# Performance work log

Hardware: AMD Instinct MI355X
Metric: run time of the kernel (lower is better)

The kernel has to match this reference:

```python
import jax, jax.numpy as jnp
import numpy as np

H = 512

def setup_inputs() -> dict:
    key = jax.random.key(0)
    ks = jax.random.split(key, 8)
    b, s, m, n, h = 8, 128, 32, 64, H
    sc = 1.0 / np.sqrt(h)
    return {
        "x": jax.random.normal(ks[0], (b, s, m, h), dtype=jnp.float32),
        "y": jax.random.normal(ks[1], (b, s, n, h), dtype=jnp.float32),
        # MultiHeadSelfAtt (additive self-attentive pooling: b*m*h -> b*h)
        "Wa1": jax.random.normal(ks[2], (h, h), dtype=jnp.float32) * sc,
        "ba1": jnp.zeros((h,), dtype=jnp.float32),
        "wa2": jax.random.normal(ks[3], (h,), dtype=jnp.float32) * sc,
        # gate Linear(2h -> h), torch layout weight: (h, 2h)
        "Wl": jax.random.normal(ks[4], (h, 2 * h), dtype=jnp.float32) * (1.0 / np.sqrt(2 * h)),
        "bl": jnp.zeros((h,), dtype=jnp.float32),
    }

def reference(x, y, Wa1, ba1, wa2, Wl, bl):
    h = x.shape[-1]
    # attentive pooling over m for every (b, s) slice: b s m h -> b s h
    scores = jnp.tanh(x @ Wa1 + ba1) @ wa2          # b s m
    attn = jax.nn.softmax(scores, axis=-1)
    pooled = jnp.einsum('bsm,bsmh->bsh', attn, x)   # b s h
    # step i (i>=1) uses pooled x at step i-1
    i_x = pooled[:, :-1]                            # b (s-1) h
    Wy, Wi = Wl[:, :h], Wl[:, h:]                   # split concat-linear
    pre = jnp.einsum('bsnh,gh->bsng', y[:, 1:], Wy) \
        + (i_x @ Wi.T + bl)[:, :, None, :]          # b (s-1) n h
    gate = jax.nn.sigmoid(pre)
    out_rest = y[:, 1:] + i_x[:, :, None, :] * gate
    return jnp.concatenate([y[:, :1], out_rest], axis=1)  # b s n h
```

## Files before the change

### kernel.cpp

```cpp
#include <hip/hip_runtime.h>
#include <cstdint>
#include <cstddef>

#define H 512
#define SEQ 128

typedef __bf16 v8bf __attribute__((ext_vector_type(8)));
typedef float v4f __attribute__((ext_vector_type(4)));
typedef unsigned short v8us __attribute__((ext_vector_type(8)));

__device__ __forceinline__ unsigned short f2bf(float f) {
    unsigned int u = __float_as_uint(f);
    u = (u + 0x7FFFu + ((u >> 16) & 1u)) >> 16;
    return (unsigned short)u;
}
__device__ __forceinline__ float bf2f(unsigned short h) {
    return __uint_as_float(((unsigned int)h) << 16);
}
__device__ __forceinline__ v8bf load_bf8(const unsigned short* p) {
    return *reinterpret_cast<const v8bf*>(p);
}
__device__ __forceinline__ float fast_tanh(float v) {
    float e = __expf(2.f * v);
    return 1.f - 2.f * __builtin_amdgcn_rcpf(e + 1.f);
}
__device__ __forceinline__ float fast_sigmoid(float v) {
    return __builtin_amdgcn_rcpf(1.f + __expf(-v));
}
__device__ __forceinline__ v8us cvt8u(float4 lo, float4 hi) {
    v8us r;
    r[0] = f2bf(lo.x); r[1] = f2bf(lo.y); r[2] = f2bf(lo.z); r[3] = f2bf(lo.w);
    r[4] = f2bf(hi.x); r[5] = f2bf(hi.y); r[6] = f2bf(hi.z); r[7] = f2bf(hi.w);
    return r;
}
__device__ __forceinline__ void gll16(const unsigned short* g, unsigned short* l) {
    __builtin_amdgcn_global_load_lds(
        (const __attribute__((address_space(1))) unsigned int*)g,
        (__attribute__((address_space(3))) unsigned int*)l, 16, 0, 0);
}


__global__ __launch_bounds__(256) void prep_kernel(
        const float* __restrict__ Wa1, const float* __restrict__ Wl,
        unsigned short* __restrict__ WyS, unsigned short* __restrict__ WiS,
        unsigned short* __restrict__ WaS) {
    int tg = blockIdx.x * 256 + threadIdx.x;
    int mat = tg >> 15;
    int idx = tg & 32767;
    int lane = idx & 63;
    int ks = (idx >> 6) & 15;
    int c = idx >> 10;
    int g = c * 16 + (lane & 15);
    int hb = ks * 32 + ((lane >> 4) << 3);
    unsigned short o[8];
    unsigned short* dst;
    if (mat == 0) {
        const float* s = Wl + (size_t)g * 1024 + hb;
#pragma unroll
        for (int j = 0; j < 8; ++j) o[j] = f2bf(s[j]);
        dst = WyS + (size_t)idx * 8;
    } else if (mat == 1) {
        const float* s = Wl + (size_t)g * 1024 + 512 + hb;
#pragma unroll
        for (int j = 0; j < 8; ++j) o[j] = f2bf(s[j]);
        dst = WiS + (size_t)idx * 8;
    } else {
#pragma unroll
        for (int j = 0; j < 8; ++j) o[j] = f2bf(Wa1[(size_t)(hb + j) * H + g]);
        dst = WaS + (size_t)idx * 8;
    }
    *reinterpret_cast<ushort4*>(dst)     = *reinterpret_cast<ushort4*>(&o[0]);
    *reinterpret_cast<ushort4*>(dst + 4) = *reinterpret_cast<ushort4*>(&o[4]);
}

__global__ __launch_bounds__(256, 4) void attn_pool_kernel(
        const float* __restrict__ x, const unsigned short* __restrict__ WaS,
        const float* __restrict__ ba1, const float* __restrict__ wa2,
        float* __restrict__ ixf, unsigned short* __restrict__ ixb) {
    __shared__ __align__(16) unsigned short Xb[32][520];
    __shared__ float attn[32];
    __shared__ float scpart[4][32];

    int bid = blockIdx.x;
    int b = bid / 127, s = bid % 127;
    int t = threadIdx.x;

    const float4* x4 = reinterpret_cast<const float4*>(x + (size_t)(b * SEQ + s) * 32 * H);
#pragma unroll
    for (int i = 0; i < 16; ++i) {
        int idx4 = t + i * 256;
        float4 v = x4[idx4];
        int e = idx4 * 4, m = e >> 9, h = e & 511;
        ushort4 o;
        o.x = f2bf(v.x); o.y = f2bf(v.y); o.z = f2bf(v.z); o.w = f2bf(v.w);
        *reinterpret_cast<ushort4*>(&Xb[m][h]) = o;
    }
    __syncthreads();

    int w = t >> 6, lane = t & 63, q = lane >> 4, c16 = lane & 15;

    v4f acc[2][8];
#pragma unroll
    for (int mi = 0; mi < 2; ++mi)
#pragma unroll
        for (int ci = 0; ci < 8; ++ci) acc[mi][ci] = (v4f){0.f, 0.f, 0.f, 0.f};

    const unsigned short* Bb = WaS + (size_t)(w * 8 * 16) * 512 + lane * 8;

#pragma unroll
    for (int ks = 0; ks < 16; ++ks) {
        v8bf a0 = load_bf8(&Xb[c16][ks * 32 + q * 8]);
        v8bf a1 = load_bf8(&Xb[16 + c16][ks * 32 + q * 8]);
#pragma unroll
        for (int ci = 0; ci < 8; ++ci) {
            v8bf bb = load_bf8(Bb + (size_t)(ci * 16 + ks) * 512);
            acc[0][ci] = __builtin_amdgcn_mfma_f32_16x16x32_bf16(a0, bb, acc[0][ci], 0, 0, 0);
            acc[1][ci] = __builtin_amdgcn_mfma_f32_16x16x32_bf16(a1, bb, acc[1][ci], 0, 0, 0);
        }
    }

    float sr[2][4] = {{0.f, 0.f, 0.f, 0.f}, {0.f, 0.f, 0.f, 0.f}};
#pragma unroll
    for (int ci = 0; ci < 8; ++ci) {
        int g = (w * 8 + ci) * 16 + c16;
        float w2 = wa2[g];
        float bv = ba1[g];
#pragma unroll
        for (int mi = 0; mi < 2; ++mi)
#pragma unroll
            for (int i = 0; i < 4; ++i)
                sr[mi][i] += w2 * fast_tanh(acc[mi][ci][i] + bv);
    }
#pragma unroll
    for (int off = 1; off < 16; off <<= 1) {
#pragma unroll
        for (int mi = 0; mi < 2; ++mi)
#pragma unroll
            for (int i = 0; i < 4; ++i) sr[mi][i] += __shfl_xor(sr[mi][i], off);
    }
    if (c16 == 0) {
#pragma unroll
        for (int mi = 0; mi < 2; ++mi)
#pragma unroll
            for (int i = 0; i < 4; ++i) scpart[w][mi * 16 + q * 4 + i] = sr[mi][i];
    }
    __syncthreads();

    if (t < 64) {
        int m = t & 31;
        float v = scpart[0][m] + scpart[1][m] + scpart[2][m] + scpart[3][m];
        float mx = v;
#pragma unroll
        for (int off = 1; off < 32; off <<= 1) mx = fmaxf(mx, __shfl_xor(mx, off));
        float e = __expf(v - mx);
        float sum = e;
#pragma unroll
        for (int off = 1; off < 32; off <<= 1) sum += __shfl_xor(sum, off);
        if (t < 32) attn[m] = e * __builtin_amdgcn_rcpf(sum);
    }
    __syncthreads();

    int h0 = t * 2;
    float p0 = 0.f, p1 = 0.f;
#pragma unroll
    for (int m = 0; m < 32; ++m) {
        float am = attn[m];
        p0 += am * bf2f(Xb[m][h0]);
        p1 += am * bf2f(Xb[m][h0 + 1]);
    }
    size_t r = (size_t)bid;
    ixf[r * H + h0] = p0;
    ixf[r * H + h0 + 1] = p1;
    ixb[r * H + h0] = f2bf(p0);
    ixb[r * H + h0 + 1] = f2bf(p1);
}

__global__ __launch_bounds__(256) void ipre_kernel(
        const unsigned short* __restrict__ ixb, const unsigned short* __restrict__ WiS,
        const float* __restrict__ bl, float* __restrict__ ipre) {
    int row16 = blockIdx.x * 16;
    int t = threadIdx.x, w = t >> 6, lane = t & 63, q = lane >> 4, c16 = lane & 15;
    int c0 = blockIdx.y * 8 + w * 2;

    v4f acc0 = {0.f, 0.f, 0.f, 0.f};
    v4f acc1 = {0.f, 0.f, 0.f, 0.f};
    const unsigned short* arow = ixb + (size_t)(row16 + c16) * H + q * 8;
#pragma unroll
    for (int ks = 0; ks < 16; ++ks) {
        v8bf a = load_bf8(arow + ks * 32);
        acc0 = __builtin_amdgcn_mfma_f32_16x16x32_bf16(
            a, load_bf8(WiS + (size_t)(c0 * 16 + ks) * 512 + lane * 8), acc0, 0, 0, 0);
        acc1 = __builtin_amdgcn_mfma_f32_16x16x32_bf16(
            a, load_bf8(WiS + (size_t)((c0 + 1) * 16 + ks) * 512 + lane * 8), acc1, 0, 0, 0);
    }
#pragma unroll
    for (int cc = 0; cc < 2; ++cc) {
        int g = (c0 + cc) * 16 + c16;
        float blv = bl[g];
        v4f a = cc ? acc1 : acc0;
#pragma unroll
        for (int i = 0; i < 4; ++i) {
            int row = row16 + q * 4 + i;
            if (row < 1016) ipre[(size_t)row * H + g] = a[i] + blv;
        }
    }
}

__global__ __launch_bounds__(512, 4) void main_kernel(
        const float* __restrict__ y, const unsigned short* __restrict__ WyS,
        const float* __restrict__ ixf, const float* __restrict__ ipre,
        float* __restrict__ out) {
    int bid0 = blockIdx.x;
    int t = threadIdx.x;

    if (bid0 >= 1016) {
        int cb = bid0 - 1016;
        int b = cb >> 1, half = cb & 1;
        size_t base = ((size_t)(b * SEQ)) * 64 * H + (size_t)half * 32 * H;
        const float4* y4 = reinterpret_cast<const float4*>(y + base);
        float4* o4 = reinterpret_cast<float4*>(out + base);
#pragma unroll
        for (int i = 0; i < 8; ++i) o4[t + i * 512] = y4[t + i * 512];
        return;
    }

    int bid = (bid0 & 7) * 127 + (bid0 >> 3);

    int rg = bid >> 1;
    int ch = bid & 1;

    __shared__ __align__(16) unsigned short Ab[2][128 * 40];
    __shared__ __align__(16) unsigned short Bb[2][16 * 512];
    __shared__ float ip_s[2][256];
    __shared__ float ix_s[2][256];

    int t0 = rg * 2;

    int arow  = t >> 2;
    int acol0 = (t & 3) * 8;
    int atid  = t0 + (arow >> 6);
    int ab    = atid / 127, asm1 = atid % 127;
    const float* yrow = y + ((size_t)(ab * SEQ + asm1 + 1) * 64 + (arow & 63)) * H;

    int w = t >> 6, lane = t & 63, q = lane >> 4, c16 = lane & 15;
    int ck0 = w * 2;
    const unsigned short* bsrc0 = WyS + (size_t)((ch * 16 + ck0) * 16) * 512 + lane * 8;
    const unsigned short* bsrc1 = WyS + (size_t)((ch * 16 + ck0 + 1) * 16) * 512 + lane * 8;

    {
        int tile = t >> 8, gl = t & 255;
        size_t rrow = (size_t)(t0 + tile) * H + ch * 256 + gl;
        ip_s[tile][gl] = ipre[rrow];
        ix_s[tile][gl] = ixf[rrow];
    }

    {
        gll16(bsrc0, &Bb[0][ck0 * 512]);
        gll16(bsrc1, &Bb[0][(ck0 + 1) * 512]);
        float4 a0 = *reinterpret_cast<const float4*>(yrow + acol0);
        float4 a1 = *reinterpret_cast<const float4*>(yrow + acol0 + 4);
        *reinterpret_cast<v8us*>(&Ab[0][arow * 40 + acol0]) = cvt8u(a0, a1);
    }
    __syncthreads();

    int wr = w >> 1;
    int wc = w & 1;

    v4f acc[2][8];
#pragma unroll
    for (int rt = 0; rt < 2; ++rt)
#pragma unroll
        for (int ci = 0; ci < 8; ++ci) acc[rt][ci] = (v4f){0.f, 0.f, 0.f, 0.f};

#pragma unroll
    for (int p = 0; p < 16; ++p) {
        const int cur = p & 1;
        float4 na0, na1;
        if (p < 15) {
            gll16(bsrc0 + (p + 1) * 512, &Bb[cur ^ 1][ck0 * 512]);
            gll16(bsrc1 + (p + 1) * 512, &Bb[cur ^ 1][(ck0 + 1) * 512]);
            na0 = *reinterpret_cast<const float4*>(yrow + (p + 1) * 32 + acol0);
            na1 = *reinterpret_cast<const float4*>(yrow + (p + 1) * 32 + acol0 + 4);
        }

        v8bf af0 = load_bf8(&Ab[cur][(wr * 32 + c16) * 40 + q * 8]);
        v8bf af1 = load_bf8(&Ab[cur][(wr * 32 + 16 + c16) * 40 + q * 8]);
#pragma unroll
        for (int ci = 0; ci < 8; ++ci) {
            v8bf bf = load_bf8(&Bb[cur][(wc * 8 + ci) * 512 + lane * 8]);
            acc[0][ci] = __builtin_amdgcn_mfma_f32_16x16x32_bf16(af0, bf, acc[0][ci], 0, 0, 0);
            acc[1][ci] = __builtin_amdgcn_mfma_f32_16x16x32_bf16(af1, bf, acc[1][ci], 0, 0, 0);
        }

        if (p < 15) {
            *reinterpret_cast<v8us*>(&Ab[cur ^ 1][arow * 40 + acol0]) = cvt8u(na0, na1);
            __syncthreads();
        }
    }

    int tb0 = t0, tb1 = t0 + 1;
    size_t obase0 = ((size_t)((tb0 / 127) * SEQ + tb0 % 127 + 1) * 64) * H;
    size_t obase1 = ((size_t)((tb1 / 127) * SEQ + tb1 % 127 + 1) * 64) * H;
    int tile = wr >> 1;
    size_t obase = tile ? obase1 : obase0;

#pragma unroll
    for (int ci = 0; ci < 8; ++ci) {
        int gl = (wc * 8 + ci) * 16 + c16;
        int g = ch * 256 + gl;
        float ip = ip_s[tile][gl];
        float ixv = ix_s[tile][gl];
#pragma unroll
        for (int rt = 0; rt < 2; ++rt) {
#pragma unroll
            for (int i = 0; i < 4; ++i) {
                int n = ((wr & 1) * 32) + rt * 16 + q * 4 + i;
                size_t off = obase + (size_t)n * H + g;
                float yv = y[off];
                float pre = acc[rt][ci][i] + ip;
                out[off] = yv + ixv * fast_sigmoid(pre);
            }
        }
    }
}

extern "C" void kernel_launch(void* const* d_in, const int* in_sizes, int n_in,
                              void* d_out, int out_size, void* d_ws, size_t ws_size,
                              hipStream_t stream) {
    const float* x   = (const float*)d_in[0];
    const float* y   = (const float*)d_in[1];
    const float* Wa1 = (const float*)d_in[2];
    const float* ba1 = (const float*)d_in[3];
    const float* wa2 = (const float*)d_in[4];
    const float* Wl  = (const float*)d_in[5];
    const float* bl  = (const float*)d_in[6];
    float* out = (float*)d_out;

    char* ws = (char*)d_ws;
    unsigned short* WyS  = (unsigned short*)(ws);
    unsigned short* WiS  = (unsigned short*)(ws + 524288);
    unsigned short* WaS  = (unsigned short*)(ws + 1048576);
    float*          ixf  = (float*)(ws + 1572864);
    unsigned short* ixb  = (unsigned short*)(ws + 3670016);
    float*          ipre = (float*)(ws + 4718592);

    hipLaunchKernelGGL(prep_kernel, dim3(384), dim3(256), 0, stream, Wa1, Wl, WyS, WiS, WaS);
    hipLaunchKernelGGL(attn_pool_kernel, dim3(1016), dim3(256), 0, stream,
                       x, WaS, ba1, wa2, ixf, ixb);
    hipLaunchKernelGGL(ipre_kernel, dim3(64, 4), dim3(256), 0, stream, ixb, WiS, bl, ipre);
    hipLaunchKernelGGL(main_kernel, dim3(1032), dim3(512), 0, stream,
                       y, WyS, ixf, ipre, out);
}
```

Measured before the change: 162.6 us.

## Stage full weight slab in LDS and feed y fragments directly from global

The main GEMM kernel now gives each block four (b,s) tiles and 128 output columns instead of two tiles and 256 columns. It loads that block's entire bf16 Wy slab (128 columns × 512 K, about 128KB) into LDS once up front. The y activations are read straight from global into registers and converted to bf16 with native casts, which removes the double-buffered A/B LDS staging and the per-step barriers. In exchange, LDS use rises enough to limit residency to roughly one block per CU, each y row is read from global by four column-chunk blocks instead of two, and the K loop has no prefetch to hide global load latency.

Result: slower. 173.2 us (+6.6%).

```diff
diff --git a/kernel.cpp b/kernel.cpp
--- a/kernel.cpp
+++ b/kernel.cpp
@@ -27,10 +27,10 @@
 __device__ __forceinline__ float fast_sigmoid(float v) {
     return __builtin_amdgcn_rcpf(1.f + __expf(-v));
 }
-__device__ __forceinline__ v8us cvt8u(float4 lo, float4 hi) {
-    v8us r;
-    r[0] = f2bf(lo.x); r[1] = f2bf(lo.y); r[2] = f2bf(lo.z); r[3] = f2bf(lo.w);
-    r[4] = f2bf(hi.x); r[5] = f2bf(hi.y); r[6] = f2bf(hi.z); r[7] = f2bf(hi.w);
+__device__ __forceinline__ v8bf cvt8(float4 lo, float4 hi) {
+    v8bf r;
+    r[0] = (__bf16)lo.x; r[1] = (__bf16)lo.y; r[2] = (__bf16)lo.z; r[3] = (__bf16)lo.w;
+    r[4] = (__bf16)hi.x; r[5] = (__bf16)hi.y; r[6] = (__bf16)hi.z; r[7] = (__bf16)hi.w;
     return r;
 }
 __device__ __forceinline__ void gll16(const unsigned short* g, unsigned short* l) {
@@ -206,7 +206,7 @@
     }
 }
 
-__global__ __launch_bounds__(512, 4) void main_kernel(
+__global__ __launch_bounds__(512, 2) void main_kernel(
         const float* __restrict__ y, const unsigned short* __restrict__ WyS,
         const float* __restrict__ ixf, const float* __restrict__ ipre,
         float* __restrict__ out) {
@@ -226,46 +226,39 @@
 
     int bid = (bid0 & 7) * 127 + (bid0 >> 3);
 
-    int rg = bid >> 1;
-    int ch = bid & 1;
-
-    __shared__ __align__(16) unsigned short Ab[2][128 * 40];
-    __shared__ __align__(16) unsigned short Bb[2][16 * 512];
-    __shared__ float ip_s[2][256];
-    __shared__ float ix_s[2][256];
-
-    int t0 = rg * 2;
-
-    int arow  = t >> 2;
-    int acol0 = (t & 3) * 8;
-    int atid  = t0 + (arow >> 6);
-    int ab    = atid / 127, asm1 = atid % 127;
-    const float* yrow = y + ((size_t)(ab * SEQ + asm1 + 1) * 64 + (arow & 63)) * H;
+    int rg = bid >> 2;
+    int ch = bid & 3;
+
+    __shared__ __align__(16) unsigned short Bs[8][16][512];
+    __shared__ float ip_s[4][128];
+    __shared__ float ix_s[4][128];
 
     int w = t >> 6, lane = t & 63, q = lane >> 4, c16 = lane & 15;
-    int ck0 = w * 2;
-    const unsigned short* bsrc0 = WyS + (size_t)((ch * 16 + ck0) * 16) * 512 + lane * 8;
-    const unsigned short* bsrc1 = WyS + (size_t)((ch * 16 + ck0 + 1) * 16) * 512 + lane * 8;
+    int t0 = rg * 4;
 
     {
-        int tile = t >> 8, gl = t & 255;
-        size_t rrow = (size_t)(t0 + tile) * H + ch * 256 + gl;
+        const unsigned short* bsrc = WyS + ((size_t)((ch * 8 + w) * 16) * 64) * 8 + lane * 8;
+#pragma unroll
+        for (int ks = 0; ks < 16; ++ks)
+            gll16(bsrc + (size_t)ks * 512, &Bs[w][ks][0]);
+    }
+    {
+        int tile = t >> 7, gl = t & 127;
+        size_t rrow = (size_t)(t0 + tile) * H + ch * 128 + gl;
         ip_s[tile][gl] = ipre[rrow];
         ix_s[tile][gl] = ixf[rrow];
     }
 
-    {
-        gll16(bsrc0, &Bb[0][ck0 * 512]);
-        gll16(bsrc1, &Bb[0][(ck0 + 1) * 512]);
-        float4 a0 = *reinterpret_cast<const float4*>(yrow + acol0);
-        float4 a1 = *reinterpret_cast<const float4*>(yrow + acol0 + 4);
-        *reinterpret_cast<v8us*>(&Ab[0][arow * 40 + acol0]) = cvt8u(a0, a1);
-    }
+    int tile = w >> 1;
+    int tb = t0 + tile;
+    int b0 = tb / 127, s0 = tb % 127 + 1;
+    size_t obase = ((size_t)(b0 * SEQ + s0) * 64) * H;
+    int n0 = (w & 1) * 32 + c16;
+    const float* yrow0 = y + obase + (size_t)n0 * H;
+    const float* yrow1 = yrow0 + 16 * H;
+
     __syncthreads();
 
-    int wr = w >> 1;
-    int wc = w & 1;
-
     v4f acc[2][8];
 #pragma unroll
     for (int rt = 0; rt < 2; ++rt)
@@ -274,47 +267,33 @@
 
 #pragma unroll
     for (int p = 0; p < 16; ++p) {
-        const int cur = p & 1;
-        float4 na0, na1;
-        if (p < 15) {
-            gll16(bsrc0 + (p + 1) * 512, &Bb[cur ^ 1][ck0 * 512]);
-            gll16(bsrc1 + (p + 1) * 512, &Bb[cur ^ 1][(ck0 + 1) * 512]);
-            na0 = *reinterpret_cast<const float4*>(yrow + (p + 1) * 32 + acol0);
-            na1 = *reinterpret_cast<const float4*>(yrow + (p + 1) * 32 + acol0 + 4);
-        }
-
-        v8bf af0 = load_bf8(&Ab[cur][(wr * 32 + c16) * 40 + q * 8]);
-        v8bf af1 = load_bf8(&Ab[cur][(wr * 32 + 16 + c16) * 40 + q * 8]);
+        const float* a0p = yrow0 + p * 32 + q * 8;
+        const float* a1p = yrow1 + p * 32 + q * 8;
+        float4 l0 = *reinterpret_cast<const float4*>(a0p);
+        float4 h0 = *reinterpret_cast<const float4*>(a0p + 4);
+        float4 l1 = *reinterpret_cast<const float4*>(a1p);
+        float4 h1 = *reinterpret_cast<const float4*>(a1p + 4);
+        v8bf af0 = cvt8(l0, h0);
+        v8bf af1 = cvt8(l1, h1);
 #pragma unroll
         for (int ci = 0; ci < 8; ++ci) {
-            v8bf bf = load_bf8(&Bb[cur][(wc * 8 + ci) * 512 + lane * 8]);
+            v8bf bf = load_bf8(&Bs[ci][p][lane * 8]);
             acc[0][ci] = __builtin_amdgcn_mfma_f32_16x16x32_bf16(af0, bf, acc[0][ci], 0, 0, 0);
             acc[1][ci] = __builtin_amdgcn_mfma_f32_16x16x32_bf16(af1, bf, acc[1][ci], 0, 0, 0);
         }
-
-        if (p < 15) {
-            *reinterpret_cast<v8us*>(&Ab[cur ^ 1][arow * 40 + acol0]) = cvt8u(na0, na1);
-            __syncthreads();
-        }
-    }
-
-    int tb0 = t0, tb1 = t0 + 1;
-    size_t obase0 = ((size_t)((tb0 / 127) * SEQ + tb0 % 127 + 1) * 64) * H;
-    size_t obase1 = ((size_t)((tb1 / 127) * SEQ + tb1 % 127 + 1) * 64) * H;
-    int tile = wr >> 1;
-    size_t obase = tile ? obase1 : obase0;
+    }
 
 #pragma unroll
     for (int ci = 0; ci < 8; ++ci) {
-        int gl = (wc * 8 + ci) * 16 + c16;
-        int g = ch * 256 + gl;
+        int gl = ci * 16 + c16;
+        int g = ch * 128 + gl;
         float ip = ip_s[tile][gl];
         float ixv = ix_s[tile][gl];
 #pragma unroll
         for (int rt = 0; rt < 2; ++rt) {
 #pragma unroll
             for (int i = 0; i < 4; ++i) {
-                int n = ((wr & 1) * 32) + rt * 16 + q * 4 + i;
+                int n = (w & 1) * 32 + rt * 16 + q * 4 + i;
                 size_t off = obase + (size_t)n * H + g;
                 float yv = y[off];
                 float pre = acc[rt][ci][i] + ip;
```
